# Optimization experiments

Measured on AMD Instinct MI355X. Metric: run time of the kernel, lower is better.

Reference implementation:

```python
import jax, jax.numpy as jnp
import numpy as np

GROUPSIZE = 128

def setup_inputs() -> dict:
    key = jax.random.key(0)
    k1, k2, k3 = jax.random.split(key, 3)
    B, S, K, O = 4, 2048, 4096, 11008
    G = K // GROUPSIZE  # 32 groups
    x = jax.random.normal(k1, (B, S, K), dtype=jnp.float32)
    # int8-valued weight stored as int32 (simulated quantized weights)
    weight = jax.random.randint(k2, (O, K), -128, 128, dtype=jnp.int32)
    # per-(out_channel, group) scales, small positive values
    scales = jax.random.uniform(k3, (O, G), dtype=jnp.float32) * 0.02 + 0.001
    return {"x": x, "weight": weight, "scales": scales}

def reference(x, weight, scales):
    O, K = weight.shape
    G = scales.shape[1]
    gs = K // G
    # groupwise dequant: w_fp[o, g, j] = int8_w[o, g, j] * scales[o, g]
    w_fp = (weight.astype(x.dtype).reshape(O, G, gs) * scales[:, :, None]).reshape(O, K)
    # F.linear: x @ w_fp.T -> [B, S, O]
    return jnp.einsum('bsk,ok->bso', x, w_fp)
```

## Files before the change

kernel.cpp:

```cpp
#include <hip/hip_runtime.h>
#include <hip/hip_bf16.h>

#define MDIM 8192
#define KDIM 4096
#define NDIM 11008
#define GDIM 32

#define BM 256
#define BN 256
#define BK 64
#define NKT (KDIM / BK)
#define MT (MDIM / BM)
#define NT (NDIM / BN)
#define NWG (MT * NT)
#define CPX (NWG / 8)

typedef __attribute__((ext_vector_type(8))) short short8;
typedef __attribute__((ext_vector_type(4))) float f32x4;
typedef __attribute__((address_space(3))) unsigned char lds_u8;

__device__ __forceinline__ unsigned short f2bf(float f) {
    unsigned int u = __float_as_uint(f);
    u += 0x7FFFu + ((u >> 16) & 1u);
    return (unsigned short)(u >> 16);
}

__device__ __forceinline__ void async_ld16(const void* g, lds_u8* l) {
    __builtin_amdgcn_global_load_lds(
        (const __attribute__((address_space(1))) void*)g,
        (__attribute__((address_space(3))) void*)l, 16, 0, 0);
}

__device__ __forceinline__ void stage_half(const unsigned short* src, lds_u8* dst) {
    async_ld16(src, dst);
    async_ld16(src + (size_t)64 * KDIM, dst + 8192);
}

#define BAR()   __builtin_amdgcn_s_barrier()
#define FENCE() asm volatile("" ::: "memory")
#define LGKM0() asm volatile("s_waitcnt lgkmcnt(0)" ::: "memory")
#define VMW(n)  asm volatile("s_waitcnt vmcnt(" #n ")" ::: "memory")
#define SP1()   __builtin_amdgcn_s_setprio(1)
#define SP0()   __builtin_amdgcn_s_setprio(0)

template<int FB>
__device__ __forceinline__ void ldA4(short8 (&a)[4][2],
                                     const unsigned short* p0,
                                     const unsigned short* p1) {
#pragma unroll
    for (int f = 0; f < 4; ++f) {
        a[f][0] = *(const short8*)(p0 + (FB + f) * 1024);
        a[f][1] = *(const short8*)(p1 + (FB + f) * 1024);
    }
}

template<int NB>
__device__ __forceinline__ void ldB2(short8 (&b)[4][2],
                                     const unsigned short* p0,
                                     const unsigned short* p1) {
#pragma unroll
    for (int n = 0; n < 2; ++n) {
        b[NB + n][0] = *(const short8*)(p0 + (NB + n) * 1024);
        b[NB + n][1] = *(const short8*)(p1 + (NB + n) * 1024);
    }
}

template<int FB, int NB>
__device__ __forceinline__ void mm16(f32x4 (&acc)[8][4],
                                     const short8 (&a)[4][2],
                                     const short8 (&b)[4][2]) {
#pragma unroll
    for (int ks = 0; ks < 2; ++ks)
#pragma unroll
        for (int f = 0; f < 4; ++f)
#pragma unroll
            for (int n = 0; n < 2; ++n)
                acc[FB + f][NB + n] = __builtin_amdgcn_mfma_f32_16x16x32_bf16(
                    a[f][ks], b[NB + n][ks], acc[FB + f][NB + n], 0, 0, 0);
}

#define XBLOCKS ((MDIM * (size_t)KDIM) / 8 / 256)
#define WBLOCKS ((NDIM * (size_t)KDIM) / 8 / 256)
__global__ __launch_bounds__(256) void prep_kernel(const float* __restrict__ x,
                                                   const int* __restrict__ w,
                                                   const float* __restrict__ sc,
                                                   unsigned short* __restrict__ xb,
                                                   unsigned short* __restrict__ wb) {
    size_t b = blockIdx.x;
    if (b < XBLOCKS) {
        size_t i = (b * 256 + threadIdx.x) * 8;
        float4 f0 = *(const float4*)(x + i);
        float4 f1 = *(const float4*)(x + i + 4);
        union { unsigned short u[8]; uint4 v; } p;
        p.u[0] = f2bf(f0.x); p.u[1] = f2bf(f0.y); p.u[2] = f2bf(f0.z); p.u[3] = f2bf(f0.w);
        p.u[4] = f2bf(f1.x); p.u[5] = f2bf(f1.y); p.u[6] = f2bf(f1.z); p.u[7] = f2bf(f1.w);
        *(uint4*)(xb + i) = p.v;
    } else {
        size_t base = ((b - XBLOCKS) * 256 + threadIdx.x) * 8;
        int o = (int)(base >> 12);
        int k = (int)(base & 4095);
        float s = sc[o * GDIM + (k >> 7)];
        int4 w0 = *(const int4*)(w + base);
        int4 w1 = *(const int4*)(w + base + 4);
        union { unsigned short u[8]; uint4 v; } p;
        p.u[0] = f2bf((float)w0.x * s); p.u[1] = f2bf((float)w0.y * s);
        p.u[2] = f2bf((float)w0.z * s); p.u[3] = f2bf((float)w0.w * s);
        p.u[4] = f2bf((float)w1.x * s); p.u[5] = f2bf((float)w1.y * s);
        p.u[6] = f2bf((float)w1.z * s); p.u[7] = f2bf((float)w1.w * s);
        *(uint4*)(wb + base) = p.v;
    }
}

__global__ __launch_bounds__(512, 2) void gemm256(const unsigned short* __restrict__ A,
                                                  const unsigned short* __restrict__ B,
                                                  float* __restrict__ C) {
    __shared__ unsigned short lds[65536];

    const int tid  = threadIdx.x;
    const int wave = tid >> 6;
    const int lane = tid & 63;
    const int wm = wave >> 2, wn = wave & 3;
    const int q  = lane >> 4;
    const int ml = lane & 15;
    const int s  = ml & 7;

    const int p    = blockIdx.x;
    const int tix  = (p & 7) * CPX + (p >> 3);
    const int bm   = tix & 31;
    const int bn   = tix >> 5;
    const int row0 = bm * BM, col0 = bn * BN;

    const int e0  = ((q    ) ^ s) * 8;
    const int e1  = ((4 + q) ^ s) * 8;
    const int rdA = wm * 8192 + ml * 64;
    const int rdB = 32768 + wn * 4096 + ml * 64;

    const int rA = tid >> 3;
    const int cS = (tid & 7) ^ (rA & 7);
    const unsigned short* gA = A + (size_t)(row0 + rA) * KDIM + cS * 8;
    const unsigned short* gB = B + (size_t)(col0 + rA) * KDIM + cS * 8;
    lds_u8* L8A = (lds_u8*)lds + tid * 16;
    lds_u8* L8B = L8A + 65536;

    stage_half(gA,                      L8A);
    stage_half(gA + (size_t)128 * KDIM, L8A + 16384);
    stage_half(gB,                      L8B);
    stage_half(gB + (size_t)128 * KDIM, L8B + 16384);
    stage_half(gB + 64,                      L8B + 32768);
    stage_half(gB + (size_t)128 * KDIM + 64, L8B + 32768 + 16384);
    const unsigned short* pAg = gA + 64;
    const unsigned short* pBg = gB + 128;
    VMW(4);
    BAR(); FENCE();

    short8 a[4][2], b[4][2];
    f32x4 acc[8][4];
    const f32x4 z = {0.f, 0.f, 0.f, 0.f};
#pragma unroll
    for (int f = 0; f < 8; ++f)
#pragma unroll
        for (int n = 0; n < 4; ++n) acc[f][n] = z;

    ldB2<0>(b, lds + rdB + e0, lds + rdB + e1);

    for (int kt = 0; kt < NKT; ++kt) {
        const int cur = kt & 1;
        const unsigned short* Lc  = lds + cur * 16384;
        const unsigned short* pA0 = Lc + rdA + e0;
        const unsigned short* pA1 = Lc + rdA + e1;
        const unsigned short* pB0 = Lc + rdB + e0;
        const unsigned short* pB1 = Lc + rdB + e1;
        const unsigned short* Ln  = lds + (cur ^ 1) * 16384;
        const unsigned short* pB0n = Ln + rdB + e0;
        const unsigned short* pB1n = Ln + rdB + e1;
        lds_u8* dA = L8A + (((kt + 1) & 1) << 15);
        lds_u8* dB = L8B + ((cur) << 15);
        const bool stA = (kt + 1 < NKT);
        const bool stB = (kt + 2 < NKT);

        ldA4<0>(a, pA0, pA1);
        if (stA) stage_half(pAg, dA);
        BAR();
        LGKM0();
        SP1();
        mm16<0, 0>(acc, a, b);
        SP0();
        BAR(); FENCE();

        ldB2<2>(b, pB0, pB1);
        if (stA) stage_half(pAg + (size_t)128 * KDIM, dA + 16384);
        BAR();
        LGKM0();
        SP1();
        mm16<0, 2>(acc, a, b);
        SP0();
        BAR(); FENCE();

        ldA4<4>(a, pA0, pA1);
        if (stB) stage_half(pBg, dB);
        BAR();
        LGKM0();
        SP1();
        mm16<4, 0>(acc, a, b);
        SP0();
        BAR(); FENCE();

        if (stB) stage_half(pBg + (size_t)128 * KDIM, dB + 16384);
        if (stB)      { VMW(4); }
        else if (stA) { VMW(0); }
        BAR(); FENCE();
        if (stA) ldB2<0>(b, pB0n, pB1n);
        SP1();
        mm16<4, 2>(acc, a, b);
        SP0();
        BAR(); FENCE();

        pAg += 64; pBg += 64;
    }

#pragma unroll
    for (int f = 0; f < 8; ++f) {
        const int r0 = row0 + wm * 128 + f * 16 + q * 4;
#pragma unroll
        for (int n = 0; n < 4; ++n) {
            const int c = col0 + wn * 64 + n * 16 + ml;
            float* Cp = C + (size_t)r0 * NDIM + c;
#pragma unroll
            for (int r = 0; r < 4; ++r) Cp[(size_t)r * NDIM] = acc[f][n][r];
        }
    }
}

__global__ __launch_bounds__(256) void gemm_fallback(const float* __restrict__ X,
                                                     const int* __restrict__ W,
                                                     const float* __restrict__ S,
                                                     float* __restrict__ C) {
    int n = blockIdx.x * 256 + threadIdx.x;
    int m = blockIdx.y;
    if (n >= NDIM) return;
    const float* xr = X + (size_t)m * KDIM;
    const int*   wr = W + (size_t)n * KDIM;
    float acc = 0.f;
    for (int g = 0; g < GDIM; ++g) {
        float s = S[n * GDIM + g];
        float part = 0.f;
        for (int k = 0; k < 128; ++k)
            part += xr[g * 128 + k] * (float)wr[g * 128 + k];
        acc += part * s;
    }
    C[(size_t)m * NDIM + n] = acc;
}

extern "C" void kernel_launch(void* const* d_in, const int* in_sizes, int n_in,
                              void* d_out, int out_size, void* d_ws, size_t ws_size,
                              hipStream_t stream) {
    const float* x  = (const float*)d_in[0];
    const int*   w  = (const int*)d_in[1];
    const float* sc = (const float*)d_in[2];
    float* out = (float*)d_out;

    const size_t bytesA = (size_t)MDIM * KDIM * 2;
    const size_t bytesB = (size_t)NDIM * KDIM * 2;

    if (ws_size >= bytesA + bytesB) {
        unsigned short* Abf = (unsigned short*)d_ws;
        unsigned short* Bbf = (unsigned short*)((char*)d_ws + bytesA);

        prep_kernel<<<(unsigned)(XBLOCKS + WBLOCKS), 256, 0, stream>>>(x, w, sc, Abf, Bbf);
        gemm256<<<NWG, 512, 0, stream>>>(Abf, Bbf, out);
    } else {
        dim3 grid((NDIM + 255) / 256, MDIM);
        gemm_fallback<<<grid, 256, 0, stream>>>(x, w, sc, out);
    }
}
```

Baseline: 1.173 ms.

## Cut per-iteration barriers and split B fragments into separate register sets

Restructures the K-loop of the bf16 MFMA GEMM. It drops from eight workgroup barriers and explicit lgkmcnt(0) waits per iteration to two barriers, letting the compiler place the LDS wait counts. Both async A-tile loads are now issued together up front, and both B-tile loads after the mid-iteration barrier. The B fragments are split into two register arrays (b1, b2), so the next tile's first B fragment can load while the second is still used by MFMAs. The aim is less stall time at barriers and more overlap of LDS reads with matrix work. The cost is that correctness now depends on careful buffer reuse ordering, and register pressure may rise.

```diff
diff --git a/kernel.cpp b/kernel.cpp
--- a/kernel.cpp
+++ b/kernel.cpp
@@ -38,7 +38,6 @@
 
 #define BAR()   __builtin_amdgcn_s_barrier()
 #define FENCE() asm volatile("" ::: "memory")
-#define LGKM0() asm volatile("s_waitcnt lgkmcnt(0)" ::: "memory")
 #define VMW(n)  asm volatile("s_waitcnt vmcnt(" #n ")" ::: "memory")
 #define SP1()   __builtin_amdgcn_s_setprio(1)
 #define SP0()   __builtin_amdgcn_s_setprio(0)
@@ -55,20 +54,20 @@
 }
 
 template<int NB>
-__device__ __forceinline__ void ldB2(short8 (&b)[4][2],
+__device__ __forceinline__ void ldB2(short8 (&bb)[2][2],
                                      const unsigned short* p0,
                                      const unsigned short* p1) {
 #pragma unroll
     for (int n = 0; n < 2; ++n) {
-        b[NB + n][0] = *(const short8*)(p0 + (NB + n) * 1024);
-        b[NB + n][1] = *(const short8*)(p1 + (NB + n) * 1024);
+        bb[n][0] = *(const short8*)(p0 + (NB + n) * 1024);
+        bb[n][1] = *(const short8*)(p1 + (NB + n) * 1024);
     }
 }
 
 template<int FB, int NB>
 __device__ __forceinline__ void mm16(f32x4 (&acc)[8][4],
                                      const short8 (&a)[4][2],
-                                     const short8 (&b)[4][2]) {
+                                     const short8 (&bb)[2][2]) {
 #pragma unroll
     for (int ks = 0; ks < 2; ++ks)
 #pragma unroll
@@ -76,7 +75,7 @@
 #pragma unroll
             for (int n = 0; n < 2; ++n)
                 acc[FB + f][NB + n] = __builtin_amdgcn_mfma_f32_16x16x32_bf16(
-                    a[f][ks], b[NB + n][ks], acc[FB + f][NB + n], 0, 0, 0);
+                    a[f][ks], bb[n][ks], acc[FB + f][NB + n], 0, 0, 0);
 }
 
 #define XBLOCKS ((MDIM * (size_t)KDIM) / 8 / 256)
@@ -153,7 +152,7 @@
     VMW(4);
     BAR(); FENCE();
 
-    short8 a[4][2], b[4][2];
+    short8 a[4][2], b1[2][2], b2[2][2];
     f32x4 acc[8][4];
     const f32x4 z = {0.f, 0.f, 0.f, 0.f};
 #pragma unroll
@@ -161,7 +160,7 @@
 #pragma unroll
         for (int n = 0; n < 4; ++n) acc[f][n] = z;
 
-    ldB2<0>(b, lds + rdB + e0, lds + rdB + e1);
+    ldB2<0>(b1, lds + rdB + e0, lds + rdB + e1);
 
     for (int kt = 0; kt < NKT; ++kt) {
         const int cur = kt & 1;
@@ -179,41 +178,33 @@
         const bool stB = (kt + 2 < NKT);
 
         ldA4<0>(a, pA0, pA1);
-        if (stA) stage_half(pAg, dA);
-        BAR();
-        LGKM0();
-        SP1();
-        mm16<0, 0>(acc, a, b);
-        SP0();
+        if (stA) {
+            stage_half(pAg, dA);
+            stage_half(pAg + (size_t)128 * KDIM, dA + 16384);
+        }
+        SP1(); mm16<0, 0>(acc, a, b1); SP0();
+
+        ldB2<2>(b2, pB0, pB1);
+        SP1(); mm16<0, 2>(acc, a, b2); SP0();
+
+        ldA4<4>(a, pA0, pA1);
+
         BAR(); FENCE();
 
-        ldB2<2>(b, pB0, pB1);
-        if (stA) stage_half(pAg + (size_t)128 * KDIM, dA + 16384);
-        BAR();
-        LGKM0();
-        SP1();
-        mm16<0, 2>(acc, a, b);
-        SP0();
-        BAR(); FENCE();
-
-        ldA4<4>(a, pA0, pA1);
-        if (stB) stage_half(pBg, dB);
-        BAR();
-        LGKM0();
-        SP1();
-        mm16<4, 0>(acc, a, b);
-        SP0();
-        BAR(); FENCE();
-
-        if (stB) stage_half(pBg + (size_t)128 * KDIM, dB + 16384);
+        if (stB) {
+            stage_half(pBg, dB);
+            stage_half(pBg + (size_t)128 * KDIM, dB + 16384);
+        }
+
+        SP1(); mm16<4, 0>(acc, a, b1); SP0();
+
         if (stB)      { VMW(4); }
         else if (stA) { VMW(0); }
         BAR(); FENCE();
-        if (stA) ldB2<0>(b, pB0n, pB1n);
-        SP1();
-        mm16<4, 2>(acc, a, b);
-        SP0();
-        BAR(); FENCE();
+
+        if (stA) ldB2<0>(b1, pB0n, pB1n);
+
+        SP1(); mm16<4, 2>(acc, a, b2); SP0();
 
         pAg += 64; pBg += 64;
     }
```

After: 1.171 ms. Within noise of the previous version (-0.1%).
